# Optimization experiments

Hardware: AMD Instinct MI355X
Metric: run time of the kernel (lower is better)

The kernel has to match this reference:

```python
import jax, jax.numpy as jnp
import numpy as np

B, S, C_IN, C_OUT = 8, 2048, 512, 512

def setup_inputs() -> dict:
    key = jax.random.key(0)
    k1, k2, k3, k4 = jax.random.split(key, 4)
    sc = 1.0 / np.sqrt(C_IN)
    return {
        "x": jax.random.normal(k1, (B, S, C_IN), dtype=jnp.float32),
        "Wq": jax.random.normal(k2, (C_OUT, C_IN), dtype=jnp.float32) * sc,
        "Wk": jax.random.normal(k3, (C_OUT, C_IN), dtype=jnp.float32) * sc,
        "Wv": jax.random.normal(k4, (C_OUT, C_IN), dtype=jnp.float32) * sc,
    }

def reference(x, Wq, Wk, Wv):
    # x: [B,S,Cin]; weights [Cout,Cin] (torch Linear convention, no bias)
    C = Wq.shape[0]
    dk = jnp.sqrt(jnp.float32(1.0) / C)  # torch: sqrt(1/out_features)
    q = jnp.einsum('bsi,oi->bso', x, Wq)
    k = jnp.einsum('bsi,oi->bso', x, Wk)
    v = jnp.einsum('bsi,oi->bso', x, Wv)
    phi_q = jax.nn.elu(q * dk) + 1.0
    phi_k = jax.nn.elu(k * dk) + 1.0
    b = x.shape[0]
    mem0 = jnp.zeros((b, C, C), x.dtype)   # running sum of phi_k v^T
    zeta0 = jnp.zeros((b, C), x.dtype)     # running sum of phi_k
    def step(carry, inp):
        mem, zeta = carry
        pq, pk, vv = inp                    # each [B,C]
        dm = pk[:, :, None] * vv[:, None, :]              # [B,C,C]
        scale = jnp.einsum('bc,bc->b', pq, pk + zeta) + 1e-5
        num = jnp.einsum('bc,bcd->bd', pq, dm + mem)
        y = num / scale[:, None]
        # state updates are under torch.no_grad -> detach
        new_mem = jax.lax.stop_gradient(mem + dm)
        new_zeta = jax.lax.stop_gradient(zeta + pk)
        return (new_mem, new_zeta), y
    xs = (phi_q.transpose(1, 0, 2), phi_k.transpose(1, 0, 2), v.transpose(1, 0, 2))
    _, ys = jax.lax.scan(step, (mem0, zeta0), xs)  # ys: [S,B,C]
    return ys.transpose(1, 0, 2)                   # [B,S,C]
```

## Files before the change

kernel.cpp:

```cpp
#include <hip/hip_runtime.h>


constexpr int Bn  = 8;
constexpr int Sn  = 2048;
constexpr int Cn  = 512;
constexpr int Tn  = 128;
constexpr int NCn = 16;
constexpr float DKf = 0.04419417382415922f;

typedef __attribute__((ext_vector_type(8))) short bf16x8;
typedef __attribute__((ext_vector_type(4))) float f32x4;

__device__ __forceinline__ unsigned short f2bf(float f) {
  unsigned u = __float_as_uint(f);
  u = (u + 0x7fffu + ((u >> 16) & 1u)) >> 16;
  return (unsigned short)u;
}
__device__ __forceinline__ float bf2f(unsigned short h) {
  return __uint_as_float(((unsigned)h) << 16);
}
__device__ __forceinline__ float phi_f(float u) {
  float s = u * DKf;
  return s > 0.0f ? s + 1.0f : __expf(s);
}

__device__ __forceinline__ void stage128x32(const unsigned short* __restrict__ g,
                                            int ld, unsigned short* lds,
                                            int wid, int lane) {
#pragma unroll
  for (int cc = 0; cc < 2; ++cc) {
    const int row = cc * 64 + wid * 16 + (lane >> 2);
    const int ks  = (lane & 3) ^ ((row >> 1) & 3);
    const unsigned short* src = g + (size_t)row * ld + ks * 8;
    unsigned short* dst = lds + (size_t)(cc * 256 + wid * 64) * 8;
    __builtin_amdgcn_global_load_lds(
        (const __attribute__((address_space(1))) void*)src,
        (__attribute__((address_space(3))) void*)dst, 16, 0, 0);
  }
}

__device__ __forceinline__ void mm_loop(const unsigned short* __restrict__ Ag, int lda,
                                        const unsigned short* __restrict__ Bg, int ldb,
                                        int nkt,
                                        unsigned short* Al, unsigned short* Bl,
                                        f32x4 acc[4][4]) {
  const int t = threadIdx.x, wid = t >> 6, lane = t & 63;
  const int wm = wid >> 1, wn = wid & 1;
  const int fr = lane & 15, kb = lane >> 4;
  stage128x32(Ag, lda, Al, wid, lane);
  stage128x32(Bg, ldb, Bl, wid, lane);
  if (nkt > 1) {
    stage128x32(Ag + 32, lda, Al + 4096, wid, lane);
    stage128x32(Bg + 32, ldb, Bl + 4096, wid, lane);
  }
  int cur = 0;
  for (int kt = 0; kt < nkt; ++kt) {
    if (kt + 2 < nkt) {
      const int nx2 = (cur + 2 >= 3) ? cur - 1 : cur + 2;
      stage128x32(Ag + (kt + 2) * 32, lda, Al + nx2 * 4096, wid, lane);
      stage128x32(Bg + (kt + 2) * 32, ldb, Bl + nx2 * 4096, wid, lane);
      asm volatile("s_waitcnt vmcnt(8)" ::: "memory");
    } else if (kt + 1 < nkt) {
      asm volatile("s_waitcnt vmcnt(4)" ::: "memory");
    } else {
      asm volatile("s_waitcnt vmcnt(0)" ::: "memory");
    }
    __builtin_amdgcn_s_barrier();
    asm volatile("" ::: "memory");
    const unsigned short* Ac = Al + cur * 4096;
    const unsigned short* Bc = Bl + cur * 4096;
    bf16x8 af[4], bf[4];
#pragma unroll
    for (int m = 0; m < 4; ++m) {
      const int r = wm * 64 + m * 16 + fr;
      af[m] = *(const bf16x8*)&Ac[r * 32 + ((kb ^ ((r >> 1) & 3)) << 3)];
    }
#pragma unroll
    for (int n = 0; n < 4; ++n) {
      const int r = wn * 64 + n * 16 + fr;
      bf[n] = *(const bf16x8*)&Bc[r * 32 + ((kb ^ ((r >> 1) & 3)) << 3)];
    }
    __builtin_amdgcn_s_setprio(1);
#pragma unroll
    for (int m = 0; m < 4; ++m)
#pragma unroll
      for (int n = 0; n < 4; ++n)
        acc[m][n] = __builtin_amdgcn_mfma_f32_16x16x32_bf16(af[m], bf[n], acc[m][n], 0, 0, 0);
    __builtin_amdgcn_s_setprio(0);
    __builtin_amdgcn_s_barrier();
    asm volatile("" ::: "memory");
    cur = (cur + 1 >= 3) ? 0 : cur + 1;
  }
}

__global__ __launch_bounds__(256) void k_cast(
    const float* __restrict__ x, const float* __restrict__ Wq,
    const float* __restrict__ Wk, const float* __restrict__ Wv,
    unsigned short* __restrict__ xb, unsigned short* __restrict__ Wb)
{
  const int bid = blockIdx.x;
  const float* src;
  unsigned short* dst;
  size_t i8;
  if (bid < 4096) {
    i8 = ((size_t)bid * 256 + threadIdx.x) * 8;
    src = x; dst = xb;
  } else {
    const size_t f = ((size_t)(bid - 4096) * 256 + threadIdx.x) * 8;
    const int z = (int)(f >> 18);
    src = (z == 0) ? Wq : (z == 1 ? Wk : Wv);
    dst = Wb + ((size_t)z << 18);
    i8 = f & ((1u << 18) - 1);
  }
  float4 a = *(const float4*)&src[i8];
  float4 b = *(const float4*)&src[i8 + 4];
  uint4 o;
  o.x = (unsigned)f2bf(a.x) | ((unsigned)f2bf(a.y) << 16);
  o.y = (unsigned)f2bf(a.z) | ((unsigned)f2bf(a.w) << 16);
  o.z = (unsigned)f2bf(b.x) | ((unsigned)f2bf(b.y) << 16);
  o.w = (unsigned)f2bf(b.z) | ((unsigned)f2bf(b.w) << 16);
  *(uint4*)&dst[i8] = o;
}

__global__ __launch_bounds__(256) void k_proj(
    const unsigned short* __restrict__ xb, const unsigned short* __restrict__ Wb,
    unsigned short* __restrict__ PQ, unsigned short* __restrict__ PK,
    unsigned short* __restrict__ PKt, unsigned short* __restrict__ Vt,
    float* __restrict__ zsum)
{
  __shared__ unsigned short Al[3 * 128 * 32], Bl[3 * 128 * 32];
  __shared__ float zbuf[2][128];
  const int bid = blockIdx.x;
  const int xcd = bid & 7, idx = bid >> 3;
  const int n = idx & 3, z = (idx >> 2) % 3, mloc = idx / 12;
  const int n0 = n * 128, m0 = (xcd * 16 + mloc) * 128;
  const int t = threadIdx.x, wid = t >> 6, lane = t & 63;
  const int wm = wid >> 1, wn = wid & 1;
  f32x4 acc[4][4];
  const f32x4 zero = {0.f, 0.f, 0.f, 0.f};
#pragma unroll
  for (int m = 0; m < 4; ++m)
#pragma unroll
    for (int nn = 0; nn < 4; ++nn) acc[m][nn] = zero;

  mm_loop(xb + (size_t)m0 * Cn, Cn,
          Wb + (size_t)z * Cn * Cn + (size_t)n0 * Cn, Cn, Cn / 32, Al, Bl, acc);

  float ps[4] = {0.f, 0.f, 0.f, 0.f};
#pragma unroll
  for (int m = 0; m < 4; ++m)
#pragma unroll
    for (int nn = 0; nn < 4; ++nn) {
      const int row0 = m0 + wm * 64 + m * 16 + ((lane >> 4) << 2);
      const int col  = n0 + wn * 64 + nn * 16 + (lane & 15);
      f32x4 v = acc[m][nn];
      if (z == 0) {
#pragma unroll
        for (int j = 0; j < 4; ++j)
          PQ[(size_t)(row0 + j) * Cn + col] = f2bf(phi_f(v[j]));
      } else if (z == 1) {
        ushort4 p;
#pragma unroll
        for (int j = 0; j < 4; ++j) {
          unsigned short u = f2bf(phi_f(v[j]));
          PK[(size_t)(row0 + j) * Cn + col] = u;
          (&p.x)[j] = u;
          ps[nn] += bf2f(u);
        }
        const int b = row0 >> 11, tq = row0 & (Sn - 1);
        *(ushort4*)&PKt[((size_t)b * Cn + col) * Sn + tq] = p;
      } else {
        ushort4 p;
#pragma unroll
        for (int j = 0; j < 4; ++j) (&p.x)[j] = f2bf(v[j]);
        const int b = row0 >> 11, tq = row0 & (Sn - 1);
        *(ushort4*)&Vt[((size_t)b * Cn + col) * Sn + tq] = p;
      }
    }

  if (z == 1) {
#pragma unroll
    for (int nn = 0; nn < 4; ++nn) {
      float v = ps[nn];
      v += __shfl_xor(v, 16); v += __shfl_xor(v, 32);
      if (lane < 16) zbuf[wm][wn * 64 + nn * 16 + lane] = v;
    }
    __syncthreads();
    if (t < 128) {
      const int b = m0 >> 11, ch = (m0 >> 7) & 15;
      zsum[((size_t)b * NCn + ch) * Cn + n0 + t] = zbuf[0][t] + zbuf[1][t];
    }
  }
}

__device__ __forceinline__ void stageA64(const unsigned short* __restrict__ g,
                                         unsigned short* lds, int wid, int lane) {
  const int row = wid * 16 + (lane >> 2);
  const int ks  = (lane & 3) ^ ((row >> 1) & 3);
  __builtin_amdgcn_global_load_lds(
      (const __attribute__((address_space(1))) void*)(g + (size_t)row * Cn + ks * 8),
      (__attribute__((address_space(3))) void*)(lds + wid * 512), 16, 0, 0);
}
__device__ __forceinline__ void stageB128(const unsigned short* __restrict__ g,
                                          unsigned short* lds, int wid, int lane) {
#pragma unroll
  for (int e = 0; e < 2; ++e) {
    const int row = e * 64 + wid * 16 + (lane >> 2);
    const int ks  = (lane & 3) ^ ((row >> 1) & 3);
    __builtin_amdgcn_global_load_lds(
        (const __attribute__((address_space(1))) void*)(g + (size_t)row * Cn + ks * 8),
        (__attribute__((address_space(3))) void*)(lds + e * 2048 + wid * 512),
        16, 0, 0);
  }
}

__global__ __launch_bounds__(256) void k_gram(
    const unsigned short* __restrict__ PQ, const unsigned short* __restrict__ PK,
    const float* __restrict__ zsum,
    unsigned short* __restrict__ Abuf, float* __restrict__ scale)
{
  __shared__ unsigned short Asl[3 * 2048], Bsl[3 * 4096];
  __shared__ float rsmem[4][64];
  __shared__ float zpl[512];
  const int b = blockIdx.z, ch = blockIdx.y, i0 = blockIdx.x * 64;
  const unsigned short* Aq = PQ + ((size_t)(b * Sn + ch * Tn + i0)) * Cn;
  const unsigned short* Bk = PK + ((size_t)(b * Sn + ch * Tn)) * Cn;
  const int t = threadIdx.x, wid = t >> 6, lane = t & 63;
  const int fr = lane & 15, kb = lane >> 4;
  f32x4 acc[4][2];
  const f32x4 zero = {0.f, 0.f, 0.f, 0.f};
#pragma unroll
  for (int m = 0; m < 4; ++m)
#pragma unroll
    for (int n = 0; n < 2; ++n) acc[m][n] = zero;

  stageA64(Aq, Asl, wid, lane);
  stageB128(Bk, Bsl, wid, lane);
  stageA64(Aq + 32, Asl + 2048, wid, lane);
  stageB128(Bk + 32, Bsl + 4096, wid, lane);
  int cur = 0;
  for (int kt = 0; kt < 16; ++kt) {
    if (kt + 2 < 16) {
      const int nx2 = (cur + 2 >= 3) ? cur - 1 : cur + 2;
      stageA64(Aq + (kt + 2) * 32, Asl + nx2 * 2048, wid, lane);
      stageB128(Bk + (kt + 2) * 32, Bsl + nx2 * 4096, wid, lane);
      asm volatile("s_waitcnt vmcnt(6)" ::: "memory");
    } else if (kt + 1 < 16) {
      asm volatile("s_waitcnt vmcnt(3)" ::: "memory");
    } else {
      asm volatile("s_waitcnt vmcnt(0)" ::: "memory");
    }
    __builtin_amdgcn_s_barrier();
    asm volatile("" ::: "memory");
    const unsigned short* Ac = Asl + cur * 2048;
    const unsigned short* Bc = Bsl + cur * 4096;
    bf16x8 af[4], bf[2];
#pragma unroll
    for (int m = 0; m < 4; ++m) {
      const int r = m * 16 + fr;
      af[m] = *(const bf16x8*)&Ac[r * 32 + ((kb ^ ((r >> 1) & 3)) << 3)];
    }
#pragma unroll
    for (int n = 0; n < 2; ++n) {
      const int c = wid * 32 + n * 16 + fr;
      bf[n] = *(const bf16x8*)&Bc[c * 32 + ((kb ^ ((c >> 1) & 3)) << 3)];
    }
    __builtin_amdgcn_s_setprio(1);
#pragma unroll
    for (int m = 0; m < 4; ++m)
#pragma unroll
      for (int n = 0; n < 2; ++n)
        acc[m][n] = __builtin_amdgcn_mfma_f32_16x16x32_bf16(af[m], bf[n], acc[m][n], 0, 0, 0);
    __builtin_amdgcn_s_setprio(0);
    __builtin_amdgcn_s_barrier();
    asm volatile("" ::: "memory");
    cur = (cur + 1 >= 3) ? 0 : cur + 1;
  }

  float rsum[4][4];
#pragma unroll
  for (int m = 0; m < 4; ++m)
#pragma unroll
    for (int j = 0; j < 4; ++j) rsum[m][j] = 0.f;
#pragma unroll
  for (int m = 0; m < 4; ++m)
#pragma unroll
    for (int n = 0; n < 2; ++n) {
      f32x4 v = acc[m][n];
#pragma unroll
      for (int j = 0; j < 4; ++j) {
        const int row_g = i0 + m * 16 + kb * 4 + j;
        const int col   = wid * 32 + n * 16 + fr;
        unsigned short u = (col <= row_g) ? f2bf(v[j]) : 0;
        Abuf[((size_t)(b * NCn + ch) * Tn + row_g) * Tn + col] = u;
        rsum[m][j] += bf2f(u);
      }
    }
#pragma unroll
  for (int m = 0; m < 4; ++m)
#pragma unroll
    for (int j = 0; j < 4; ++j) {
      float r = rsum[m][j];
      r += __shfl_xor(r, 1); r += __shfl_xor(r, 2);
      r += __shfl_xor(r, 4); r += __shfl_xor(r, 8);
      if (fr == 0) rsmem[wid][m * 16 + kb * 4 + j] = r;
    }
#pragma unroll
  for (int e = 0; e < 2; ++e) {
    const int c = t + e * 256;
    float s = 0.f;
    for (int ch2 = 0; ch2 < ch; ++ch2)
      s += zsum[((size_t)b * NCn + ch2) * Cn + c];
    zpl[c] = s;
  }
  __syncthreads();
  const int row = t >> 2, q4 = (t & 3) * 128;
  const unsigned short* pq = Aq + (size_t)row * Cn + q4;
  float dacc = 0.f;
  for (int i = 0; i < 128; i += 8) {
    uint4 q = *(const uint4*)(pq + i);
    dacc += bf2f((unsigned short)(q.x & 0xffff)) * zpl[q4 + i + 0]
          + bf2f((unsigned short)(q.x >> 16))    * zpl[q4 + i + 1]
          + bf2f((unsigned short)(q.y & 0xffff)) * zpl[q4 + i + 2]
          + bf2f((unsigned short)(q.y >> 16))    * zpl[q4 + i + 3]
          + bf2f((unsigned short)(q.z & 0xffff)) * zpl[q4 + i + 4]
          + bf2f((unsigned short)(q.z >> 16))    * zpl[q4 + i + 5]
          + bf2f((unsigned short)(q.w & 0xffff)) * zpl[q4 + i + 6]
          + bf2f((unsigned short)(q.w >> 16))    * zpl[q4 + i + 7];
  }
  dacc += __shfl_xor(dacc, 1);
  dacc += __shfl_xor(dacc, 2);
  if ((t & 3) == 0)
    scale[(size_t)b * Sn + ch * Tn + i0 + row] =
        rsmem[0][row] + rsmem[1][row] + rsmem[2][row] + rsmem[3][row] + dacc + 1e-5f;
}

__device__ __forceinline__ void stage64x128(const unsigned short* __restrict__ g,
                                            int ld, unsigned short* lds,
                                            int wid, int lane) {
#pragma unroll
  for (int i = 0; i < 4; ++i) {
    const int row = wid * 16 + i * 4 + (lane >> 4);
    const int s   = (lane & 15) ^ (row & 7);
    const unsigned short* src = g + (size_t)row * ld + s * 8;
    unsigned short* dst = lds + (size_t)(wid * 16 + i * 4) * 128;
    __builtin_amdgcn_global_load_lds(
        (const __attribute__((address_space(1))) void*)src,
        (__attribute__((address_space(3))) void*)dst, 16, 0, 0);
  }
}

__global__ __launch_bounds__(256) void k_kvp(
    const unsigned short* __restrict__ PKt, const unsigned short* __restrict__ Vt,
    unsigned short* __restrict__ Mpre)
{
  __shared__ unsigned short Al[2 * 64 * 128], Bl[2 * 64 * 128];
  const int bid = blockIdx.x;
  const int b = bid & 7, idx = bid >> 3;
  const int d0 = (idx & 7) * 64, c0 = (idx >> 3) * 64;
  const int t = threadIdx.x, wid = t >> 6, lane = t & 63;
  const int wm = wid >> 1, wn = wid & 1;
  const int fr = lane & 15, kb = lane >> 4;
  f32x4 acc[2][2];
  const f32x4 zero = {0.f, 0.f, 0.f, 0.f};
#pragma unroll
  for (int m = 0; m < 2; ++m)
#pragma unroll
    for (int n = 0; n < 2; ++n) acc[m][n] = zero;
  const unsigned short* Ag = PKt + ((size_t)b * Cn + c0) * Sn;
  const unsigned short* Bg = Vt  + ((size_t)b * Cn + d0) * Sn;
  stage64x128(Ag, Sn, Al, wid, lane);
  stage64x128(Bg, Sn, Bl, wid, lane);
  int cur = 0;
  for (int ch = 0; ch < NCn; ++ch) {
    const int nxt = cur ^ 1;
    if (ch + 1 < NCn) {
      stage64x128(Ag + (ch + 1) * Tn, Sn, Al + nxt * 8192, wid, lane);
      stage64x128(Bg + (ch + 1) * Tn, Sn, Bl + nxt * 8192, wid, lane);
      asm volatile("s_waitcnt vmcnt(8)" ::: "memory");
    } else {
      asm volatile("s_waitcnt vmcnt(0)" ::: "memory");
    }
    __builtin_amdgcn_s_barrier();
    asm volatile("" ::: "memory");
    if (ch > 0) {
#pragma unroll
      for (int m = 0; m < 2; ++m)
#pragma unroll
        for (int n = 0; n < 2; ++n) {
          const int c_row = c0 + wm * 32 + m * 16 + (kb << 2);
          const int d     = d0 + wn * 32 + n * 16 + fr;
          ushort4 p;
#pragma unroll
          for (int j = 0; j < 4; ++j) (&p.x)[j] = f2bf(acc[m][n][j]);
          *(ushort4*)&Mpre[((size_t)(b * NCn + ch) * Cn + d) * Cn + c_row] = p;
        }
    }
    const unsigned short* Ac = Al + cur * 8192;
    const unsigned short* Bc = Bl + cur * 8192;
    __builtin_amdgcn_s_setprio(1);
#pragma unroll
    for (int kt = 0; kt < 4; ++kt) {
      bf16x8 af[2], bf[2];
#pragma unroll
      for (int m = 0; m < 2; ++m) {
        const int r = wm * 32 + m * 16 + fr;
        af[m] = *(const bf16x8*)&Ac[r * 128 + (((kt * 4 + kb) ^ (r & 7)) << 3)];
      }
#pragma unroll
      for (int n = 0; n < 2; ++n) {
        const int r = wn * 32 + n * 16 + fr;
        bf[n] = *(const bf16x8*)&Bc[r * 128 + (((kt * 4 + kb) ^ (r & 7)) << 3)];
      }
#pragma unroll
      for (int m = 0; m < 2; ++m)
#pragma unroll
        for (int n = 0; n < 2; ++n)
          acc[m][n] = __builtin_amdgcn_mfma_f32_16x16x32_bf16(af[m], bf[n], acc[m][n], 0, 0, 0);
    }
    __builtin_amdgcn_s_setprio(0);
    __builtin_amdgcn_s_barrier();
    asm volatile("" ::: "memory");
    cur = nxt;
  }
}

__global__ __launch_bounds__(256) void k_avinter(
    const unsigned short* __restrict__ Abuf, const unsigned short* __restrict__ Vt,
    const unsigned short* __restrict__ PQ, const unsigned short* __restrict__ Mpre,
    const float* __restrict__ scale, float* __restrict__ out)
{
  __shared__ unsigned short Al[3 * 128 * 32], Bl[3 * 128 * 32];
  const int bid = blockIdx.x;
  const int logical = (bid & 7) * 64 + (bid >> 3);
  const int d0 = (logical & 3) * 128;
  const int ch = (logical >> 2) & 15;
  const int b  = logical >> 6;
  const int t0 = ch * Tn;
  const int t = threadIdx.x, wid = t >> 6, lane = t & 63;
  const int wm = wid >> 1, wn = wid & 1;
  const int fr = lane & 15, kb = lane >> 4;
  f32x4 acc[4][4];
  const f32x4 zero = {0.f, 0.f, 0.f, 0.f};
#pragma unroll
  for (int m = 0; m < 4; ++m)
#pragma unroll
    for (int n = 0; n < 4; ++n) acc[m][n] = zero;

  const unsigned short* Aintra = Abuf + (size_t)(b * NCn + ch) * Tn * Tn;
  const unsigned short* Bintra = Vt + ((size_t)b * Cn + d0) * Sn + t0;
  const unsigned short* Ainter = PQ + ((size_t)b * Sn + t0) * Cn;
  const unsigned short* Binter = Mpre + ((size_t)(b * NCn + ch) * Cn + d0) * Cn;
  auto srcA = [&](int kt) { return (kt < 4) ? Aintra + kt * 32 : Ainter + (kt - 4) * 32; };
  auto srcB = [&](int kt) { return (kt < 4) ? Bintra + kt * 32 : Binter + (kt - 4) * 32; };
  auto ldA  = [&](int kt) { return (kt < 4) ? Tn : Cn; };
  auto ldB  = [&](int kt) { return (kt < 4) ? Sn : Cn; };
  const int nkt = (ch > 0) ? 20 : 4;

  stage128x32(srcA(0), ldA(0), Al, wid, lane);
  stage128x32(srcB(0), ldB(0), Bl, wid, lane);
  stage128x32(srcA(1), ldA(1), Al + 4096, wid, lane);
  stage128x32(srcB(1), ldB(1), Bl + 4096, wid, lane);
  int cur = 0;
  for (int kt = 0; kt < nkt; ++kt) {
    if (kt + 2 < nkt) {
      const int nx2 = (cur + 2 >= 3) ? cur - 1 : cur + 2;
      stage128x32(srcA(kt + 2), ldA(kt + 2), Al + nx2 * 4096, wid, lane);
      stage128x32(srcB(kt + 2), ldB(kt + 2), Bl + nx2 * 4096, wid, lane);
      asm volatile("s_waitcnt vmcnt(8)" ::: "memory");
    } else if (kt + 1 < nkt) {
      asm volatile("s_waitcnt vmcnt(4)" ::: "memory");
    } else {
      asm volatile("s_waitcnt vmcnt(0)" ::: "memory");
    }
    __builtin_amdgcn_s_barrier();
    asm volatile("" ::: "memory");
    const unsigned short* Ac = Al + cur * 4096;
    const unsigned short* Bc = Bl + cur * 4096;
    bf16x8 af[4], bf[4];
#pragma unroll
    for (int m = 0; m < 4; ++m) {
      const int r = wm * 64 + m * 16 + fr;
      af[m] = *(const bf16x8*)&Ac[r * 32 + ((kb ^ ((r >> 1) & 3)) << 3)];
    }
#pragma unroll
    for (int n = 0; n < 4; ++n) {
      const int r = wn * 64 + n * 16 + fr;
      bf[n] = *(const bf16x8*)&Bc[r * 32 + ((kb ^ ((r >> 1) & 3)) << 3)];
    }
    __builtin_amdgcn_s_setprio(1);
#pragma unroll
    for (int m = 0; m < 4; ++m)
#pragma unroll
      for (int n = 0; n < 4; ++n)
        acc[m][n] = __builtin_amdgcn_mfma_f32_16x16x32_bf16(af[m], bf[n], acc[m][n], 0, 0, 0);
    __builtin_amdgcn_s_setprio(0);
    __builtin_amdgcn_s_barrier();
    asm volatile("" ::: "memory");
    cur = (cur + 1 >= 3) ? 0 : cur + 1;
  }

#pragma unroll
  for (int m = 0; m < 4; ++m)
#pragma unroll
    for (int n = 0; n < 4; ++n) {
      const int row0 = t0 + wm * 64 + m * 16 + ((lane >> 4) << 2);
      const int col  = d0 + wn * 64 + n * 16 + (lane & 15);
      f32x4 v = acc[m][n];
#pragma unroll
      for (int j = 0; j < 4; ++j) {
        const size_t sidx = (size_t)b * Sn + row0 + j;
        out[sidx * Cn + col] = v[j] / scale[sidx];
      }
    }
}

extern "C" void kernel_launch(void* const* d_in, const int* in_sizes, int n_in,
                              void* d_out, int out_size, void* d_ws, size_t ws_size,
                              hipStream_t stream)
{
  const float* x  = (const float*)d_in[0];
  const float* Wq = (const float*)d_in[1];
  const float* Wk = (const float*)d_in[2];
  const float* Wv = (const float*)d_in[3];
  float* out = (float*)d_out;

  unsigned short* xb   = (unsigned short*)d_ws;
  unsigned short* Wb   = xb   + (size_t)Bn * Sn * Cn;
  unsigned short* PQ   = Wb   + (size_t)3 * Cn * Cn;
  unsigned short* PK   = PQ   + (size_t)Bn * Sn * Cn;
  unsigned short* PKt  = PK   + (size_t)Bn * Sn * Cn;
  unsigned short* Vt   = PKt  + (size_t)Bn * Sn * Cn;
  unsigned short* Abuf = Vt   + (size_t)Bn * Sn * Cn;
  unsigned short* Mpre = Abuf + (size_t)Bn * NCn * Tn * Tn;
  float* scale = (float*)(Mpre + (size_t)Bn * NCn * Cn * Cn);
  float* zsum  = scale + (size_t)Bn * Sn;
  (void)ws_size; (void)in_sizes; (void)n_in; (void)out_size;

  hipLaunchKernelGGL(k_cast, dim3(4096 + 384), dim3(256), 0, stream, x, Wq, Wk, Wv, xb, Wb);
  hipLaunchKernelGGL(k_proj, dim3(1536), dim3(256), 0, stream, xb, Wb, PQ, PK, PKt, Vt, zsum);
  hipLaunchKernelGGL(k_gram, dim3(2, NCn, Bn), dim3(256), 0, stream, PQ, PK, zsum, Abuf, scale);
  hipLaunchKernelGGL(k_kvp, dim3(512), dim3(256), 0, stream, PKt, Vt, Mpre);
  hipLaunchKernelGGL(k_avinter, dim3(512), dim3(256), 0, stream, Abuf, Vt, PQ, Mpre, scale, out);
}
```

Baseline: 125.1 us.

## Enlarge projection tiles to 256x128 and merge gram and kv-prefix kernels

```diff
diff --git a/kernel.cpp b/kernel.cpp
--- a/kernel.cpp
+++ b/kernel.cpp
@@ -22,75 +22,6 @@
 __device__ __forceinline__ float phi_f(float u) {
   float s = u * DKf;
   return s > 0.0f ? s + 1.0f : __expf(s);
-}
-
-__device__ __forceinline__ void stage128x32(const unsigned short* __restrict__ g,
-                                            int ld, unsigned short* lds,
-                                            int wid, int lane) {
-#pragma unroll
-  for (int cc = 0; cc < 2; ++cc) {
-    const int row = cc * 64 + wid * 16 + (lane >> 2);
-    const int ks  = (lane & 3) ^ ((row >> 1) & 3);
-    const unsigned short* src = g + (size_t)row * ld + ks * 8;
-    unsigned short* dst = lds + (size_t)(cc * 256 + wid * 64) * 8;
-    __builtin_amdgcn_global_load_lds(
-        (const __attribute__((address_space(1))) void*)src,
-        (__attribute__((address_space(3))) void*)dst, 16, 0, 0);
-  }
-}
-
-__device__ __forceinline__ void mm_loop(const unsigned short* __restrict__ Ag, int lda,
-                                        const unsigned short* __restrict__ Bg, int ldb,
-                                        int nkt,
-                                        unsigned short* Al, unsigned short* Bl,
-                                        f32x4 acc[4][4]) {
-  const int t = threadIdx.x, wid = t >> 6, lane = t & 63;
-  const int wm = wid >> 1, wn = wid & 1;
-  const int fr = lane & 15, kb = lane >> 4;
-  stage128x32(Ag, lda, Al, wid, lane);
-  stage128x32(Bg, ldb, Bl, wid, lane);
-  if (nkt > 1) {
-    stage128x32(Ag + 32, lda, Al + 4096, wid, lane);
-    stage128x32(Bg + 32, ldb, Bl + 4096, wid, lane);
-  }
-  int cur = 0;
-  for (int kt = 0; kt < nkt; ++kt) {
-    if (kt + 2 < nkt) {
-      const int nx2 = (cur + 2 >= 3) ? cur - 1 : cur + 2;
-      stage128x32(Ag + (kt + 2) * 32, lda, Al + nx2 * 4096, wid, lane);
-      stage128x32(Bg + (kt + 2) * 32, ldb, Bl + nx2 * 4096, wid, lane);
-      asm volatile("s_waitcnt vmcnt(8)" ::: "memory");
-    } else if (kt + 1 < nkt) {
-      asm volatile("s_waitcnt vmcnt(4)" ::: "memory");
-    } else {
-      asm volatile("s_waitcnt vmcnt(0)" ::: "memory");
-    }
-    __builtin_amdgcn_s_barrier();
-    asm volatile("" ::: "memory");
-    const unsigned short* Ac = Al + cur * 4096;
-    const unsigned short* Bc = Bl + cur * 4096;
-    bf16x8 af[4], bf[4];
-#pragma unroll
-    for (int m = 0; m < 4; ++m) {
-      const int r = wm * 64 + m * 16 + fr;
-      af[m] = *(const bf16x8*)&Ac[r * 32 + ((kb ^ ((r >> 1) & 3)) << 3)];
-    }
-#pragma unroll
-    for (int n = 0; n < 4; ++n) {
-      const int r = wn * 64 + n * 16 + fr;
-      bf[n] = *(const bf16x8*)&Bc[r * 32 + ((kb ^ ((r >> 1) & 3)) << 3)];
-    }
-    __builtin_amdgcn_s_setprio(1);
-#pragma unroll
-    for (int m = 0; m < 4; ++m)
-#pragma unroll
-      for (int n = 0; n < 4; ++n)
-        acc[m][n] = __builtin_amdgcn_mfma_f32_16x16x32_bf16(af[m], bf[n], acc[m][n], 0, 0, 0);
-    __builtin_amdgcn_s_setprio(0);
-    __builtin_amdgcn_s_barrier();
-    asm volatile("" ::: "memory");
-    cur = (cur + 1 >= 3) ? 0 : cur + 1;
-  }
 }
 
 __global__ __launch_bounds__(256) void k_cast(
@@ -122,20 +53,42 @@
   *(uint4*)&dst[i8] = o;
 }
 
-__global__ __launch_bounds__(256) void k_proj(
+__device__ __forceinline__ void stageA256(const unsigned short* __restrict__ g,
+                                          unsigned short* lds, int wid, int lane) {
+#pragma unroll
+  for (int cc = 0; cc < 2; ++cc) {
+    const int row = cc * 128 + wid * 16 + (lane >> 2);
+    const int ks  = (lane & 3) ^ ((row >> 1) & 3);
+    __builtin_amdgcn_global_load_lds(
+        (const __attribute__((address_space(1))) void*)(g + (size_t)row * Cn + ks * 8),
+        (__attribute__((address_space(3))) void*)(lds + (cc * 128 + wid * 16) * 32),
+        16, 0, 0);
+  }
+}
+__device__ __forceinline__ void stageB128w8(const unsigned short* __restrict__ g,
+                                            unsigned short* lds, int wid, int lane) {
+  const int row = wid * 16 + (lane >> 2);
+  const int ks  = (lane & 3) ^ ((row >> 1) & 3);
+  __builtin_amdgcn_global_load_lds(
+      (const __attribute__((address_space(1))) void*)(g + (size_t)row * Cn + ks * 8),
+      (__attribute__((address_space(3))) void*)(lds + (wid * 16) * 32), 16, 0, 0);
+}
+
+__global__ __launch_bounds__(512) void k_proj(
     const unsigned short* __restrict__ xb, const unsigned short* __restrict__ Wb,
     unsigned short* __restrict__ PQ, unsigned short* __restrict__ PK,
     unsigned short* __restrict__ PKt, unsigned short* __restrict__ Vt,
     float* __restrict__ zsum)
 {
-  __shared__ unsigned short Al[3 * 128 * 32], Bl[3 * 128 * 32];
-  __shared__ float zbuf[2][128];
+  __shared__ unsigned short Al[3 * 8192], Bl[3 * 4096];
+  __shared__ float zbuf[4][128];
   const int bid = blockIdx.x;
   const int xcd = bid & 7, idx = bid >> 3;
   const int n = idx & 3, z = (idx >> 2) % 3, mloc = idx / 12;
-  const int n0 = n * 128, m0 = (xcd * 16 + mloc) * 128;
+  const int n0 = n * 128, m0 = (xcd * 8 + mloc) * 256;
   const int t = threadIdx.x, wid = t >> 6, lane = t & 63;
   const int wm = wid >> 1, wn = wid & 1;
+  const int fr = lane & 15, kb = lane >> 4;
   f32x4 acc[4][4];
   const f32x4 zero = {0.f, 0.f, 0.f, 0.f};
 #pragma unroll
@@ -143,8 +96,51 @@
 #pragma unroll
     for (int nn = 0; nn < 4; ++nn) acc[m][nn] = zero;
 
-  mm_loop(xb + (size_t)m0 * Cn, Cn,
-          Wb + (size_t)z * Cn * Cn + (size_t)n0 * Cn, Cn, Cn / 32, Al, Bl, acc);
+  const unsigned short* Ag = xb + (size_t)m0 * Cn;
+  const unsigned short* Bg = Wb + (size_t)z * Cn * Cn + (size_t)n0 * Cn;
+
+  stageA256(Ag, Al, wid, lane);
+  stageB128w8(Bg, Bl, wid, lane);
+  stageA256(Ag + 32, Al + 8192, wid, lane);
+  stageB128w8(Bg + 32, Bl + 4096, wid, lane);
+  int cur = 0;
+  for (int kt = 0; kt < 16; ++kt) {
+    if (kt + 2 < 16) {
+      const int nx2 = (cur + 2 >= 3) ? cur - 1 : cur + 2;
+      stageA256(Ag + (kt + 2) * 32, Al + nx2 * 8192, wid, lane);
+      stageB128w8(Bg + (kt + 2) * 32, Bl + nx2 * 4096, wid, lane);
+      asm volatile("s_waitcnt vmcnt(6)" ::: "memory");
+    } else if (kt + 1 < 16) {
+      asm volatile("s_waitcnt vmcnt(3)" ::: "memory");
+    } else {
+      asm volatile("s_waitcnt vmcnt(0)" ::: "memory");
+    }
+    __builtin_amdgcn_s_barrier();
+    asm volatile("" ::: "memory");
+    const unsigned short* Ac = Al + cur * 8192;
+    const unsigned short* Bc = Bl + cur * 4096;
+    bf16x8 af[4], bf[4];
+#pragma unroll
+    for (int m = 0; m < 4; ++m) {
+      const int r = wm * 64 + m * 16 + fr;
+      af[m] = *(const bf16x8*)&Ac[r * 32 + ((kb ^ ((r >> 1) & 3)) << 3)];
+    }
+#pragma unroll
+    for (int nn = 0; nn < 4; ++nn) {
+      const int r = wn * 64 + nn * 16 + fr;
+      bf[nn] = *(const bf16x8*)&Bc[r * 32 + ((kb ^ ((r >> 1) & 3)) << 3)];
+    }
+    __builtin_amdgcn_s_setprio(1);
+#pragma unroll
+    for (int m = 0; m < 4; ++m)
+#pragma unroll
+      for (int nn = 0; nn < 4; ++nn)
+        acc[m][nn] = __builtin_amdgcn_mfma_f32_16x16x32_bf16(af[m], bf[nn], acc[m][nn], 0, 0, 0);
+    __builtin_amdgcn_s_setprio(0);
+    __builtin_amdgcn_s_barrier();
+    asm volatile("" ::: "memory");
+    cur = (cur + 1 >= 3) ? 0 : cur + 1;
+  }
 
   float ps[4] = {0.f, 0.f, 0.f, 0.f};
 #pragma unroll
@@ -152,7 +148,7 @@
 #pragma unroll
     for (int nn = 0; nn < 4; ++nn) {
       const int row0 = m0 + wm * 64 + m * 16 + ((lane >> 4) << 2);
-      const int col  = n0 + wn * 64 + nn * 16 + (lane & 15);
+      const int col  = n0 + wn * 64 + nn * 16 + fr;
       f32x4 v = acc[m][nn];
       if (z == 0) {
 #pragma unroll
@@ -186,9 +182,11 @@
       if (lane < 16) zbuf[wm][wn * 64 + nn * 16 + lane] = v;
     }
     __syncthreads();
-    if (t < 128) {
-      const int b = m0 >> 11, ch = (m0 >> 7) & 15;
-      zsum[((size_t)b * NCn + ch) * Cn + n0 + t] = zbuf[0][t] + zbuf[1][t];
+    if (t < 256) {
+      const int c = t >> 7, colI = t & 127;
+      const int b = m0 >> 11, ch = ((m0 >> 7) & 15) + c;
+      zsum[((size_t)b * NCn + ch) * Cn + n0 + colI] =
+          zbuf[2 * c][colI] + zbuf[2 * c + 1][colI];
     }
   }
 }
@@ -212,127 +210,6 @@
         (__attribute__((address_space(3))) void*)(lds + e * 2048 + wid * 512),
         16, 0, 0);
   }
-}
-
-__global__ __launch_bounds__(256) void k_gram(
-    const unsigned short* __restrict__ PQ, const unsigned short* __restrict__ PK,
-    const float* __restrict__ zsum,
-    unsigned short* __restrict__ Abuf, float* __restrict__ scale)
-{
-  __shared__ unsigned short Asl[3 * 2048], Bsl[3 * 4096];
-  __shared__ float rsmem[4][64];
-  __shared__ float zpl[512];
-  const int b = blockIdx.z, ch = blockIdx.y, i0 = blockIdx.x * 64;
-  const unsigned short* Aq = PQ + ((size_t)(b * Sn + ch * Tn + i0)) * Cn;
-  const unsigned short* Bk = PK + ((size_t)(b * Sn + ch * Tn)) * Cn;
-  const int t = threadIdx.x, wid = t >> 6, lane = t & 63;
-  const int fr = lane & 15, kb = lane >> 4;
-  f32x4 acc[4][2];
-  const f32x4 zero = {0.f, 0.f, 0.f, 0.f};
-#pragma unroll
-  for (int m = 0; m < 4; ++m)
-#pragma unroll
-    for (int n = 0; n < 2; ++n) acc[m][n] = zero;
-
-  stageA64(Aq, Asl, wid, lane);
-  stageB128(Bk, Bsl, wid, lane);
-  stageA64(Aq + 32, Asl + 2048, wid, lane);
-  stageB128(Bk + 32, Bsl + 4096, wid, lane);
-  int cur = 0;
-  for (int kt = 0; kt < 16; ++kt) {
-    if (kt + 2 < 16) {
-      const int nx2 = (cur + 2 >= 3) ? cur - 1 : cur + 2;
-      stageA64(Aq + (kt + 2) * 32, Asl + nx2 * 2048, wid, lane);
-      stageB128(Bk + (kt + 2) * 32, Bsl + nx2 * 4096, wid, lane);
-      asm volatile("s_waitcnt vmcnt(6)" ::: "memory");
-    } else if (kt + 1 < 16) {
-      asm volatile("s_waitcnt vmcnt(3)" ::: "memory");
-    } else {
-      asm volatile("s_waitcnt vmcnt(0)" ::: "memory");
-    }
-    __builtin_amdgcn_s_barrier();
-    asm volatile("" ::: "memory");
-    const unsigned short* Ac = Asl + cur * 2048;
-    const unsigned short* Bc = Bsl + cur * 4096;
-    bf16x8 af[4], bf[2];
-#pragma unroll
-    for (int m = 0; m < 4; ++m) {
-      const int r = m * 16 + fr;
-      af[m] = *(const bf16x8*)&Ac[r * 32 + ((kb ^ ((r >> 1) & 3)) << 3)];
-    }
-#pragma unroll
-    for (int n = 0; n < 2; ++n) {
-      const int c = wid * 32 + n * 16 + fr;
-      bf[n] = *(const bf16x8*)&Bc[c * 32 + ((kb ^ ((c >> 1) & 3)) << 3)];
-    }
-    __builtin_amdgcn_s_setprio(1);
-#pragma unroll
-    for (int m = 0; m < 4; ++m)
-#pragma unroll
-      for (int n = 0; n < 2; ++n)
-        acc[m][n] = __builtin_amdgcn_mfma_f32_16x16x32_bf16(af[m], bf[n], acc[m][n], 0, 0, 0);
-    __builtin_amdgcn_s_setprio(0);
-    __builtin_amdgcn_s_barrier();
-    asm volatile("" ::: "memory");
-    cur = (cur + 1 >= 3) ? 0 : cur + 1;
-  }
-
-  float rsum[4][4];
-#pragma unroll
-  for (int m = 0; m < 4; ++m)
-#pragma unroll
-    for (int j = 0; j < 4; ++j) rsum[m][j] = 0.f;
-#pragma unroll
-  for (int m = 0; m < 4; ++m)
-#pragma unroll
-    for (int n = 0; n < 2; ++n) {
-      f32x4 v = acc[m][n];
-#pragma unroll
-      for (int j = 0; j < 4; ++j) {
-        const int row_g = i0 + m * 16 + kb * 4 + j;
-        const int col   = wid * 32 + n * 16 + fr;
-        unsigned short u = (col <= row_g) ? f2bf(v[j]) : 0;
-        Abuf[((size_t)(b * NCn + ch) * Tn + row_g) * Tn + col] = u;
-        rsum[m][j] += bf2f(u);
-      }
-    }
-#pragma unroll
-  for (int m = 0; m < 4; ++m)
-#pragma unroll
-    for (int j = 0; j < 4; ++j) {
-      float r = rsum[m][j];
-      r += __shfl_xor(r, 1); r += __shfl_xor(r, 2);
-      r += __shfl_xor(r, 4); r += __shfl_xor(r, 8);
-      if (fr == 0) rsmem[wid][m * 16 + kb * 4 + j] = r;
-    }
-#pragma unroll
-  for (int e = 0; e < 2; ++e) {
-    const int c = t + e * 256;
-    float s = 0.f;
-    for (int ch2 = 0; ch2 < ch; ++ch2)
-      s += zsum[((size_t)b * NCn + ch2) * Cn + c];
-    zpl[c] = s;
-  }
-  __syncthreads();
-  const int row = t >> 2, q4 = (t & 3) * 128;
-  const unsigned short* pq = Aq + (size_t)row * Cn + q4;
-  float dacc = 0.f;
-  for (int i = 0; i < 128; i += 8) {
-    uint4 q = *(const uint4*)(pq + i);
-    dacc += bf2f((unsigned short)(q.x & 0xffff)) * zpl[q4 + i + 0]
-          + bf2f((unsigned short)(q.x >> 16))    * zpl[q4 + i + 1]
-          + bf2f((unsigned short)(q.y & 0xffff)) * zpl[q4 + i + 2]
-          + bf2f((unsigned short)(q.y >> 16))    * zpl[q4 + i + 3]
-          + bf2f((unsigned short)(q.z & 0xffff)) * zpl[q4 + i + 4]
-          + bf2f((unsigned short)(q.z >> 16))    * zpl[q4 + i + 5]
-          + bf2f((unsigned short)(q.w & 0xffff)) * zpl[q4 + i + 6]
-          + bf2f((unsigned short)(q.w >> 16))    * zpl[q4 + i + 7];
-  }
-  dacc += __shfl_xor(dacc, 1);
-  dacc += __shfl_xor(dacc, 2);
-  if ((t & 3) == 0)
-    scale[(size_t)b * Sn + ch * Tn + i0 + row] =
-        rsmem[0][row] + rsmem[1][row] + rsmem[2][row] + rsmem[3][row] + dacc + 1e-5f;
 }
 
 __device__ __forceinline__ void stage64x128(const unsigned short* __restrict__ g,
@@ -350,78 +227,216 @@
   }
 }
 
-__global__ __launch_bounds__(256) void k_kvp(
+__global__ __launch_bounds__(256) void k_gk(
+    const unsigned short* __restrict__ PQ, const unsigned short* __restrict__ PK,
+    const float* __restrict__ zsum,
+    unsigned short* __restrict__ Abuf, float* __restrict__ scale,
     const unsigned short* __restrict__ PKt, const unsigned short* __restrict__ Vt,
     unsigned short* __restrict__ Mpre)
 {
-  __shared__ unsigned short Al[2 * 64 * 128], Bl[2 * 64 * 128];
-  const int bid = blockIdx.x;
-  const int b = bid & 7, idx = bid >> 3;
-  const int d0 = (idx & 7) * 64, c0 = (idx >> 3) * 64;
+  __shared__ unsigned short smem[32768];
   const int t = threadIdx.x, wid = t >> 6, lane = t & 63;
-  const int wm = wid >> 1, wn = wid & 1;
   const int fr = lane & 15, kb = lane >> 4;
-  f32x4 acc[2][2];
   const f32x4 zero = {0.f, 0.f, 0.f, 0.f};
-#pragma unroll
-  for (int m = 0; m < 2; ++m)
-#pragma unroll
-    for (int n = 0; n < 2; ++n) acc[m][n] = zero;
-  const unsigned short* Ag = PKt + ((size_t)b * Cn + c0) * Sn;
-  const unsigned short* Bg = Vt  + ((size_t)b * Cn + d0) * Sn;
-  stage64x128(Ag, Sn, Al, wid, lane);
-  stage64x128(Bg, Sn, Bl, wid, lane);
-  int cur = 0;
-  for (int ch = 0; ch < NCn; ++ch) {
-    const int nxt = cur ^ 1;
-    if (ch + 1 < NCn) {
-      stage64x128(Ag + (ch + 1) * Tn, Sn, Al + nxt * 8192, wid, lane);
-      stage64x128(Bg + (ch + 1) * Tn, Sn, Bl + nxt * 8192, wid, lane);
-      asm volatile("s_waitcnt vmcnt(8)" ::: "memory");
-    } else {
-      asm volatile("s_waitcnt vmcnt(0)" ::: "memory");
-    }
-    __builtin_amdgcn_s_barrier();
-    asm volatile("" ::: "memory");
-    if (ch > 0) {
-#pragma unroll
-      for (int m = 0; m < 2; ++m)
+
+  if (blockIdx.x < 512) {
+    unsigned short* Al = smem;
+    unsigned short* Bl = smem + 16384;
+    const int bid = blockIdx.x;
+    const int b = bid & 7, idx = bid >> 3;
+    const int d0 = (idx & 7) * 64, c0 = (idx >> 3) * 64;
+    const int wm = wid >> 1, wn = wid & 1;
+    f32x4 acc[2][2];
+#pragma unroll
+    for (int m = 0; m < 2; ++m)
+#pragma unroll
+      for (int n = 0; n < 2; ++n) acc[m][n] = zero;
+    const unsigned short* Ag = PKt + ((size_t)b * Cn + c0) * Sn;
+    const unsigned short* Bg = Vt  + ((size_t)b * Cn + d0) * Sn;
+    stage64x128(Ag, Sn, Al, wid, lane);
+    stage64x128(Bg, Sn, Bl, wid, lane);
+    int cur = 0;
+    for (int ch = 0; ch < NCn; ++ch) {
+      const int nxt = cur ^ 1;
+      if (ch + 1 < NCn) {
+        stage64x128(Ag + (ch + 1) * Tn, Sn, Al + nxt * 8192, wid, lane);
+        stage64x128(Bg + (ch + 1) * Tn, Sn, Bl + nxt * 8192, wid, lane);
+        asm volatile("s_waitcnt vmcnt(8)" ::: "memory");
+      } else {
+        asm volatile("s_waitcnt vmcnt(0)" ::: "memory");
+      }
+      __builtin_amdgcn_s_barrier();
+      asm volatile("" ::: "memory");
+      if (ch > 0) {
+#pragma unroll
+        for (int m = 0; m < 2; ++m)
+#pragma unroll
+          for (int n = 0; n < 2; ++n) {
+            const int c_row = c0 + wm * 32 + m * 16 + (kb << 2);
+            const int d     = d0 + wn * 32 + n * 16 + fr;
+            ushort4 p;
+#pragma unroll
+            for (int j = 0; j < 4; ++j) (&p.x)[j] = f2bf(acc[m][n][j]);
+            *(ushort4*)&Mpre[((size_t)(b * NCn + ch) * Cn + d) * Cn + c_row] = p;
+          }
+      }
+      const unsigned short* Ac = Al + cur * 8192;
+      const unsigned short* Bc = Bl + cur * 8192;
+      __builtin_amdgcn_s_setprio(1);
+#pragma unroll
+      for (int kt = 0; kt < 4; ++kt) {
+        bf16x8 af[2], bf[2];
+#pragma unroll
+        for (int m = 0; m < 2; ++m) {
+          const int r = wm * 32 + m * 16 + fr;
+          af[m] = *(const bf16x8*)&Ac[r * 128 + (((kt * 4 + kb) ^ (r & 7)) << 3)];
+        }
 #pragma unroll
         for (int n = 0; n < 2; ++n) {
-          const int c_row = c0 + wm * 32 + m * 16 + (kb << 2);
-          const int d     = d0 + wn * 32 + n * 16 + fr;
-          ushort4 p;
-#pragma unroll
-          for (int j = 0; j < 4; ++j) (&p.x)[j] = f2bf(acc[m][n][j]);
-          *(ushort4*)&Mpre[((size_t)(b * NCn + ch) * Cn + d) * Cn + c_row] = p;
+          const int r = wn * 32 + n * 16 + fr;
+          bf[n] = *(const bf16x8*)&Bc[r * 128 + (((kt * 4 + kb) ^ (r & 7)) << 3)];
         }
-    }
-    const unsigned short* Ac = Al + cur * 8192;
-    const unsigned short* Bc = Bl + cur * 8192;
-    __builtin_amdgcn_s_setprio(1);
-#pragma unroll
-    for (int kt = 0; kt < 4; ++kt) {
-      bf16x8 af[2], bf[2];
-#pragma unroll
-      for (int m = 0; m < 2; ++m) {
-        const int r = wm * 32 + m * 16 + fr;
-        af[m] = *(const bf16x8*)&Ac[r * 128 + (((kt * 4 + kb) ^ (r & 7)) << 3)];
+#pragma unroll
+        for (int m = 0; m < 2; ++m)
+#pragma unroll
+          for (int n = 0; n < 2; ++n)
+            acc[m][n] = __builtin_amdgcn_mfma_f32_16x16x32_bf16(af[m], bf[n], acc[m][n], 0, 0, 0);
+      }
+      __builtin_amdgcn_s_setprio(0);
+      __builtin_amdgcn_s_barrier();
+      asm volatile("" ::: "memory");
+      cur = nxt;
+    }
+  } else {
+    unsigned short* Asl = smem;
+    unsigned short* Bsl = smem + 6144;
+    float* rsmem = (float*)(smem + 18432);
+    float* zpl   = rsmem + 256;
+    const int g = blockIdx.x - 512;
+    const int i0 = (g & 1) * 64, ch = (g >> 1) & 15, b = g >> 5;
+    const unsigned short* Aq = PQ + ((size_t)(b * Sn + ch * Tn + i0)) * Cn;
+    const unsigned short* Bk = PK + ((size_t)(b * Sn + ch * Tn)) * Cn;
+    f32x4 acc[4][2];
+#pragma unroll
+    for (int m = 0; m < 4; ++m)
+#pragma unroll
+      for (int n = 0; n < 2; ++n) acc[m][n] = zero;
+
+    stageA64(Aq, Asl, wid, lane);
+    stageB128(Bk, Bsl, wid, lane);
+    stageA64(Aq + 32, Asl + 2048, wid, lane);
+    stageB128(Bk + 32, Bsl + 4096, wid, lane);
+    int cur = 0;
+    for (int kt = 0; kt < 16; ++kt) {
+      if (kt + 2 < 16) {
+        const int nx2 = (cur + 2 >= 3) ? cur - 1 : cur + 2;
+        stageA64(Aq + (kt + 2) * 32, Asl + nx2 * 2048, wid, lane);
+        stageB128(Bk + (kt + 2) * 32, Bsl + nx2 * 4096, wid, lane);
+        asm volatile("s_waitcnt vmcnt(6)" ::: "memory");
+      } else if (kt + 1 < 16) {
+        asm volatile("s_waitcnt vmcnt(3)" ::: "memory");
+      } else {
+        asm volatile("s_waitcnt vmcnt(0)" ::: "memory");
+      }
+      __builtin_amdgcn_s_barrier();
+      asm volatile("" ::: "memory");
+      const unsigned short* Ac = Asl + cur * 2048;
+      const unsigned short* Bc = Bsl + cur * 4096;
+      bf16x8 af[4], bf[2];
+#pragma unroll
+      for (int m = 0; m < 4; ++m) {
+        const int r = m * 16 + fr;
+        af[m] = *(const bf16x8*)&Ac[r * 32 + ((kb ^ ((r >> 1) & 3)) << 3)];
       }
 #pragma unroll
       for (int n = 0; n < 2; ++n) {
-        const int r = wn * 32 + n * 16 + fr;
-        bf[n] = *(const bf16x8*)&Bc[r * 128 + (((kt * 4 + kb) ^ (r & 7)) << 3)];
-      }
-#pragma unroll
-      for (int m = 0; m < 2; ++m)
+        const int c = wid * 32 + n * 16 + fr;
+        bf[n] = *(const bf16x8*)&Bc[c * 32 + ((kb ^ ((c >> 1) & 3)) << 3)];
+      }
+      __builtin_amdgcn_s_setprio(1);
+#pragma unroll
+      for (int m = 0; m < 4; ++m)
 #pragma unroll
         for (int n = 0; n < 2; ++n)
           acc[m][n] = __builtin_amdgcn_mfma_f32_16x16x32_bf16(af[m], bf[n], acc[m][n], 0, 0, 0);
-    }
-    __builtin_amdgcn_s_setprio(0);
-    __builtin_amdgcn_s_barrier();
-    asm volatile("" ::: "memory");
-    cur = nxt;
+      __builtin_amdgcn_s_setprio(0);
+      __builtin_amdgcn_s_barrier();
+      asm volatile("" ::: "memory");
+      cur = (cur + 1 >= 3) ? 0 : cur + 1;
+    }
+
+    float rsum[4][4];
+#pragma unroll
+    for (int m = 0; m < 4; ++m)
+#pragma unroll
+      for (int j = 0; j < 4; ++j) rsum[m][j] = 0.f;
+#pragma unroll
+    for (int m = 0; m < 4; ++m)
+#pragma unroll
+      for (int n = 0; n < 2; ++n) {
+        f32x4 v = acc[m][n];
+#pragma unroll
+        for (int j = 0; j < 4; ++j) {
+          const int row_g = i0 + m * 16 + kb * 4 + j;
+          const int col   = wid * 32 + n * 16 + fr;
+          unsigned short u = (col <= row_g) ? f2bf(v[j]) : 0;
+          Abuf[((size_t)(b * NCn + ch) * Tn + row_g) * Tn + col] = u;
+          rsum[m][j] += bf2f(u);
+        }
+      }
+#pragma unroll
+    for (int m = 0; m < 4; ++m)
+#pragma unroll
+      for (int j = 0; j < 4; ++j) {
+        float r = rsum[m][j];
+        r += __shfl_xor(r, 1); r += __shfl_xor(r, 2);
+        r += __shfl_xor(r, 4); r += __shfl_xor(r, 8);
+        if (fr == 0) rsmem[wid * 64 + m * 16 + kb * 4 + j] = r;
+      }
+#pragma unroll
+    for (int e = 0; e < 2; ++e) {
+      const int c = t + e * 256;
+      float s = 0.f;
+      for (int ch2 = 0; ch2 < ch; ++ch2)
+        s += zsum[((size_t)b * NCn + ch2) * Cn + c];
+      zpl[c] = s;
+    }
+    __syncthreads();
+    const int row = t >> 2, q4 = (t & 3) * 128;
+    const unsigned short* pq = Aq + (size_t)row * Cn + q4;
+    float dacc = 0.f;
+    for (int i = 0; i < 128; i += 8) {
+      uint4 q = *(const uint4*)(pq + i);
+      dacc += bf2f((unsigned short)(q.x & 0xffff)) * zpl[q4 + i + 0]
+            + bf2f((unsigned short)(q.x >> 16))    * zpl[q4 + i + 1]
+            + bf2f((unsigned short)(q.y & 0xffff)) * zpl[q4 + i + 2]
+            + bf2f((unsigned short)(q.y >> 16))    * zpl[q4 + i + 3]
+            + bf2f((unsigned short)(q.z & 0xffff)) * zpl[q4 + i + 4]
+            + bf2f((unsigned short)(q.z >> 16))    * zpl[q4 + i + 5]
+            + bf2f((unsigned short)(q.w & 0xffff)) * zpl[q4 + i + 6]
+            + bf2f((unsigned short)(q.w >> 16))    * zpl[q4 + i + 7];
+    }
+    dacc += __shfl_xor(dacc, 1);
+    dacc += __shfl_xor(dacc, 2);
+    if ((t & 3) == 0)
+      scale[(size_t)b * Sn + ch * Tn + i0 + row] =
+          rsmem[0 * 64 + row] + rsmem[1 * 64 + row] +
+          rsmem[2 * 64 + row] + rsmem[3 * 64 + row] + dacc + 1e-5f;
+  }
+}
+
+__device__ __forceinline__ void stage128x32(const unsigned short* __restrict__ g,
+                                            int ld, unsigned short* lds,
+                                            int wid, int lane) {
+#pragma unroll
+  for (int cc = 0; cc < 2; ++cc) {
+    const int row = cc * 64 + wid * 16 + (lane >> 2);
+    const int ks  = (lane & 3) ^ ((row >> 1) & 3);
+    const unsigned short* src = g + (size_t)row * ld + ks * 8;
+    unsigned short* dst = lds + (size_t)(cc * 256 + wid * 64) * 8;
+    __builtin_amdgcn_global_load_lds(
+        (const __attribute__((address_space(1))) void*)src,
+        (__attribute__((address_space(3))) void*)dst, 16, 0, 0);
   }
 }
 
@@ -538,8 +553,8 @@
   (void)ws_size; (void)in_sizes; (void)n_in; (void)out_size;
 
   hipLaunchKernelGGL(k_cast, dim3(4096 + 384), dim3(256), 0, stream, x, Wq, Wk, Wv, xb, Wb);
-  hipLaunchKernelGGL(k_proj, dim3(1536), dim3(256), 0, stream, xb, Wb, PQ, PK, PKt, Vt, zsum);
-  hipLaunchKernelGGL(k_gram, dim3(2, NCn, Bn), dim3(256), 0, stream, PQ, PK, zsum, Abuf, scale);
-  hipLaunchKernelGGL(k_kvp, dim3(512), dim3(256), 0, stream, PKt, Vt, Mpre);
+  hipLaunchKernelGGL(k_proj, dim3(768), dim3(512), 0, stream, xb, Wb, PQ, PK, PKt, Vt, zsum);
+  hipLaunchKernelGGL(k_gk, dim3(768), dim3(256), 0, stream,
+                     PQ, PK, zsum, Abuf, scale, PKt, Vt, Mpre);
   hipLaunchKernelGGL(k_avinter, dim3(512), dim3(256), 0, stream, Abuf, Vt, PQ, Mpre, scale, out);
 }
```

New measurement: 124.9 us. About the same (-0.1%).
